# Kernel tuning notes

Measured on AMD Instinct MI355X. Metric: run time of the kernel, lower is better.

Reference implementation:

```python
import jax, jax.numpy as jnp
import numpy as np

N_ATOMS = 4096
N_NEIGH = 32
IN_F = 128
HID = 256
OUT_F = 128
N_SPECIES = 64


def setup_inputs() -> dict:
    key = jax.random.key(0)
    k1, k2, k3, k4, k5, k6 = jax.random.split(key, 6)
    # kaiming-uniform-ish init scales (exact init doesn't matter for correctness testing)
    s1 = 1.0 / np.sqrt(IN_F)
    s2 = 1.0 / np.sqrt(HID)
    return {
        "features": jax.random.normal(k1, (N_ATOMS, N_NEIGH, IN_F), dtype=jnp.float32),
        "species_idx": jax.random.randint(k2, (N_ATOMS,), 0, N_SPECIES, dtype=jnp.int64 if jax.config.jax_enable_x64 else jnp.int32),
        "W1": jax.random.uniform(k3, (N_SPECIES, HID, IN_F), jnp.float32, -s1, s1),
        "b1": jax.random.uniform(k4, (N_SPECIES, HID), jnp.float32, -s1, s1),
        "W2": jax.random.uniform(k5, (N_SPECIES, OUT_F, HID), jnp.float32, -s2, s2),
        "b2": jax.random.uniform(k6, (N_SPECIES, OUT_F), jnp.float32, -s2, s2),
    }


def reference(features, species_idx, W1, b1, W2, b2):
    # Per-atom species-conditioned 2-layer MLP with SiLU after the hidden layer.
    # features: (A, N, in); W[idx]: (A, out, in) gathered per atom (as in torch W[idx]).
    x = jnp.einsum("ani,ahi->anh", features, W1[species_idx]) + b1[species_idx][:, None, :]
    x = jax.nn.silu(x)
    x = jnp.einsum("anh,aoh->ano", x, W2[species_idx]) + b2[species_idx][:, None, :]
    return x  # (A, N, out)
```

## Files before the change

kernel.cpp:

```cpp
#include <hip/hip_runtime.h>

typedef __attribute__((ext_vector_type(8))) short short8;
typedef __attribute__((ext_vector_type(4))) float f32x4;

#define N_ATOMS 4096
#define N_NEIGH 32
#define IN_F 128
#define HID 256
#define OUT_F 128
#define N_SPECIES 64

__device__ __forceinline__ unsigned short f2bf(float f) {
  unsigned u = __float_as_uint(f);
  u += 0x7FFF + ((u >> 16) & 1);
  return (unsigned short)(u >> 16);
}
struct HL { short h, l; };
__device__ __forceinline__ HL split2(float v) {
  unsigned u = __float_as_uint(v);
  float lo = v - __uint_as_float(u & 0xFFFF0000u);
  HL o;
  o.h = (short)(u >> 16);
  o.l = (short)(__float_as_uint(lo) >> 16);
  return o;
}

__global__ __launch_bounds__(256) void prep_kernel(
    const float* __restrict__ W1, const float* __restrict__ W2,
    const int* __restrict__ sp_idx,
    unsigned short* __restrict__ w1h, unsigned short* __restrict__ w2h,
    int* __restrict__ atom_order, int* __restrict__ sp_off, int* __restrict__ sp_cnt) {
  const int t = threadIdx.x;
  if (blockIdx.x == 0) {
    __shared__ int cnt[N_SPECIES], off[N_SPECIES], cur[N_SPECIES];
    if (t < N_SPECIES) cnt[t] = 0;
    __syncthreads();
    for (int a = t; a < N_ATOMS; a += 256) atomicAdd(&cnt[sp_idx[a]], 1);
    __syncthreads();
    if (t == 0) {
      int o = 0;
      for (int s = 0; s < N_SPECIES; ++s) { off[s] = o; cur[s] = o; o += cnt[s]; }
    }
    __syncthreads();
    for (int a = t; a < N_ATOMS; a += 256) {
      int s = sp_idx[a];
      atom_order[atomicAdd(&cur[s], 1)] = a;
    }
    if (t < N_SPECIES) { sp_off[t] = off[t]; sp_cnt[t] = cnt[t]; }
    return;
  }
  const int NV = (N_SPECIES * HID * IN_F) / 4;
  const int nsplit = (gridDim.x - 1) * 256;
  for (int v = (blockIdx.x - 1) * 256 + t; v < 2 * NV; v += nsplit) {
    const float4* src; unsigned short* dh; int j;
    if (v < NV) { src = (const float4*)W1; dh = w1h; j = v; }
    else        { src = (const float4*)W2; dh = w2h; j = v - NV; }
    float4 f = src[j];
    ushort4 h;
    h.x = f2bf(f.x); h.y = f2bf(f.y); h.z = f2bf(f.z); h.w = f2bf(f.w);
    ((ushort4*)dh)[j] = h;
  }
}

__global__ __launch_bounds__(512, 2) void mlp_kernel(
    const float* __restrict__ feat,
    const float* __restrict__ b1g, const float* __restrict__ b2g,
    const unsigned short* __restrict__ w1h, const unsigned short* __restrict__ w2h,
    const int* __restrict__ atom_order, const int* __restrict__ sp_off,
    const int* __restrict__ sp_cnt,
    float* __restrict__ out) {
  extern __shared__ char smem[];
  char* LW1 = smem;
  char* LW2 = smem + 65536;

  const int bid = blockIdx.x;
  const int s = (bid & 7) * 8 + (bid >> 5);
  const int p = (bid >> 3) & 3;
  const int tid = threadIdx.x;
  const int wave = tid >> 6, lane = tid & 63;
  const int q = lane >> 4, r = lane & 15;

  {
    const char* gw1 = (const char*)w1h + (long)s * (HID * IN_F * 2);
    const char* gw2 = (const char*)w2h + (long)s * (OUT_F * HID * 2);
#pragma unroll
    for (int it = 0; it < 8; ++it) {
      const int d = it * 8192 + tid * 16;
      const int h = d >> 8, w = d & 255;
      const int src = h * (IN_F * 2) + (w ^ ((h & 7) << 4));
      __builtin_amdgcn_global_load_lds(
          (const __attribute__((address_space(1))) unsigned int*)(gw1 + src),
          (__attribute__((address_space(3))) unsigned int*)(LW1 + d), 16, 0, 0);
    }
#pragma unroll
    for (int it = 0; it < 8; ++it) {
      const int d = it * 8192 + tid * 16;
      const int o = d >> 9, w = d & 511;
      const int src = o * (HID * 2) + (w ^ ((o & 7) << 4));
      __builtin_amdgcn_global_load_lds(
          (const __attribute__((address_space(1))) unsigned int*)(gw2 + src),
          (__attribute__((address_space(3))) unsigned int*)(LW2 + d), 16, 0, 0);
    }
  }

  const int c = sp_cnt[s], base = sp_off[s];
  const int begin = base + (p * c) / 4;
  const int end   = base + ((p + 1) * c) / 4;

  float b2v[8];
#pragma unroll
  for (int ot = 0; ot < 8; ++ot) b2v[ot] = b2g[s * OUT_F + 16 * ot + r];
  const float* b1s = b1g + s * HID;

  char* lxw = smem + 131072 + wave * 4096;
  const int swz = (r & 7) << 4;

  float4 R[16];
  auto ISSUE = [&](int atom) {
    const float* fb = feat + (long)atom * (N_NEIGH * IN_F);
#pragma unroll
    for (int nt = 0; nt < 2; ++nt)
#pragma unroll
      for (int ks = 0; ks < 4; ++ks) {
        const float* ptr = fb + (16 * nt + r) * IN_F + 32 * ks + 8 * q;
        R[nt * 8 + ks * 2]     = *(const float4*)ptr;
        R[nt * 8 + ks * 2 + 1] = *(const float4*)(ptr + 4);
      }
  };

  int idx = begin + wave;
  int a_cur = 0;
  if (idx < end) { a_cur = atom_order[idx]; ISSUE(a_cur); }

  asm volatile("s_waitcnt vmcnt(0)" ::: "memory");
  __syncthreads();

  while (idx < end) {
    short8 fh[2][4], fl[2][4];
#pragma unroll
    for (int nt = 0; nt < 2; ++nt)
#pragma unroll
      for (int ks = 0; ks < 4; ++ks) {
        float4 v0 = R[nt * 8 + ks * 2];
        float4 v1 = R[nt * 8 + ks * 2 + 1];
        float vv[8] = {v0.x, v0.y, v0.z, v0.w, v1.x, v1.y, v1.z, v1.w};
        short8 h8, l8;
#pragma unroll
        for (int j = 0; j < 8; ++j) {
          HL hl = split2(vv[j]);
          h8[j] = hl.h;
          l8[j] = hl.l;
        }
        fh[nt][ks] = h8;
        fl[nt][ks] = l8;
      }
    const int atom_here = a_cur;
    const int nidx = idx + 8;
    if (nidx < end) { a_cur = atom_order[nidx]; ISSUE(a_cur); }

    f32x4 oacc[2][8] = {};
    for (int hc = 0; hc < 8; ++hc) {
      f32x4 xacc[2][2] = {};
#pragma unroll
      for (int ks = 0; ks < 4; ++ks) {
        const int ib = ((32 * ks + 8 * q) * 2) ^ swz;
#pragma unroll
        for (int ht = 0; ht < 2; ++ht) {
          const int row = 32 * hc + 16 * ht + r;
          short8 bh = *(const short8*)(LW1 + row * 256 + ib);
          xacc[0][ht] = __builtin_amdgcn_mfma_f32_16x16x32_bf16(fh[0][ks], bh, xacc[0][ht], 0, 0, 0);
          xacc[1][ht] = __builtin_amdgcn_mfma_f32_16x16x32_bf16(fh[1][ks], bh, xacc[1][ht], 0, 0, 0);
          xacc[0][ht] = __builtin_amdgcn_mfma_f32_16x16x32_bf16(fl[0][ks], bh, xacc[0][ht], 0, 0, 0);
          xacc[1][ht] = __builtin_amdgcn_mfma_f32_16x16x32_bf16(fl[1][ks], bh, xacc[1][ht], 0, 0, 0);
        }
      }
#pragma unroll
      for (int ht = 0; ht < 2; ++ht) {
        const float b1v = b1s[hc * 32 + 16 * ht + r];
#pragma unroll
        for (int nt = 0; nt < 2; ++nt)
#pragma unroll
          for (int i = 0; i < 4; ++i) {
            const int n = 16 * nt + 4 * q + i;
            float v = xacc[nt][ht][i] + b1v;
            v = v * __builtin_amdgcn_rcpf(1.0f + __expf(-v));
            const int byte = n * 128 + (((16 * ht + r) * 4) ^ ((n & 7) << 4));
            *(float*)(lxw + byte) = v;
          }
      }
      short8 ah[2], al[2];
#pragma unroll
      for (int nt = 0; nt < 2; ++nt) {
        const int n = 16 * nt + r;
        float4 v0 = *(const float4*)(lxw + n * 128 + ((32 * q) ^ swz));
        float4 v1 = *(const float4*)(lxw + n * 128 + ((32 * q + 16) ^ swz));
        float vv[8] = {v0.x, v0.y, v0.z, v0.w, v1.x, v1.y, v1.z, v1.w};
        short8 h8, l8;
#pragma unroll
        for (int j = 0; j < 8; ++j) {
          HL hl = split2(vv[j]);
          h8[j] = hl.h;
          l8[j] = hl.l;
        }
        ah[nt] = h8;
        al[nt] = l8;
      }
      const int kb = ((32 * hc + 8 * q) * 2) ^ swz;
#pragma unroll
      for (int ot = 0; ot < 8; ++ot) {
        const int row = 16 * ot + r;
        short8 bw = *(const short8*)(LW2 + row * 512 + kb);
        oacc[0][ot] = __builtin_amdgcn_mfma_f32_16x16x32_bf16(ah[0], bw, oacc[0][ot], 0, 0, 0);
        oacc[1][ot] = __builtin_amdgcn_mfma_f32_16x16x32_bf16(ah[1], bw, oacc[1][ot], 0, 0, 0);
        oacc[0][ot] = __builtin_amdgcn_mfma_f32_16x16x32_bf16(al[0], bw, oacc[0][ot], 0, 0, 0);
        oacc[1][ot] = __builtin_amdgcn_mfma_f32_16x16x32_bf16(al[1], bw, oacc[1][ot], 0, 0, 0);
      }
    }

    float* ob = out + (long)atom_here * (N_NEIGH * OUT_F);
#pragma unroll
    for (int ot = 0; ot < 8; ++ot)
#pragma unroll
      for (int nt = 0; nt < 2; ++nt)
#pragma unroll
        for (int i = 0; i < 4; ++i) {
          ob[(16 * nt + 4 * q + i) * OUT_F + 16 * ot + r] = oacc[nt][ot][i] + b2v[ot];
        }

    idx = nidx;
  }
}

extern "C" void kernel_launch(void* const* d_in, const int* in_sizes, int n_in,
                              void* d_out, int out_size, void* d_ws, size_t ws_size,
                              hipStream_t stream) {
  const float* feat = (const float*)d_in[0];
  const int* sp     = (const int*)d_in[1];
  const float* W1   = (const float*)d_in[2];
  const float* b1   = (const float*)d_in[3];
  const float* W2   = (const float*)d_in[4];
  const float* b2   = (const float*)d_in[5];
  float* out = (float*)d_out;

  char* ws = (char*)d_ws;
  unsigned short* w1h = (unsigned short*)(ws + 0);
  unsigned short* w2h = (unsigned short*)(ws + 4194304);
  int* atom_order = (int*)(ws + 8388608);
  int* sp_off     = (int*)(ws + 8388608 + 16384);
  int* sp_cnt     = (int*)(ws + 8388608 + 16384 + 256);

  hipFuncSetAttribute((const void*)mlp_kernel,
                      hipFuncAttributeMaxDynamicSharedMemorySize, 163840);

  hipLaunchKernelGGL(prep_kernel, dim3(1025), dim3(256), 0, stream,
                     W1, W2, sp, w1h, w2h, atom_order, sp_off, sp_cnt);
  hipLaunchKernelGGL(mlp_kernel, dim3(256), dim3(512), 163840, stream,
                     feat, b1, b2, w1h, w2h, atom_order, sp_off, sp_cnt, out);
}
```

Baseline: 198.0 us.

## Swap MFMA operand roles to keep hidden activations in registers and coalesce stores

The MFMA operands are transposed so weights become the A operand and features the B operand. The W1 rows are permuted at LDS load time so the layer-1 accumulator layout lines up with the B-operand layout layer 2 needs. This removes the LDS round trip for SiLU activations. Output is staged through a per-wave LDS slab so stores go out as coalesced float4 writes. The software prefetch of the next atom's features into registers is dropped, which exposes global load latency in exchange for fewer registers.

```diff
diff --git a/kernel.cpp b/kernel.cpp
--- a/kernel.cpp
+++ b/kernel.cpp
@@ -86,8 +86,11 @@
 #pragma unroll
     for (int it = 0; it < 8; ++it) {
       const int d = it * 8192 + tid * 16;
-      const int h = d >> 8, w = d & 255;
-      const int src = h * (IN_F * 2) + (w ^ ((h & 7) << 4));
+      const int pos = d >> 8, wb = d & 255;
+      const int pl = pos & 31;
+      const int hl = ((pl >> 2) & 3) * 8 + ((pl >> 4) & 1) * 4 + (pl & 3);
+      const int srow = (pos & ~31) + hl;
+      const int src = srow * (IN_F * 2) + (wb ^ ((pos & 7) << 4));
       __builtin_amdgcn_global_load_lds(
           (const __attribute__((address_space(1))) unsigned int*)(gw1 + src),
           (__attribute__((address_space(3))) unsigned int*)(LW1 + d), 16, 0, 0);
@@ -95,8 +98,8 @@
 #pragma unroll
     for (int it = 0; it < 8; ++it) {
       const int d = it * 8192 + tid * 16;
-      const int o = d >> 9, w = d & 511;
-      const int src = o * (HID * 2) + (w ^ ((o & 7) << 4));
+      const int o = d >> 9, wb = d & 511;
+      const int src = o * (HID * 2) + (wb ^ ((o & 7) << 4));
       __builtin_amdgcn_global_load_lds(
           (const __attribute__((address_space(1))) unsigned int*)(gw2 + src),
           (__attribute__((address_space(3))) unsigned int*)(LW2 + d), 16, 0, 0);
@@ -107,58 +110,42 @@
   const int begin = base + (p * c) / 4;
   const int end   = base + ((p + 1) * c) / 4;
 
-  float b2v[8];
-#pragma unroll
-  for (int ot = 0; ot < 8; ++ot) b2v[ot] = b2g[s * OUT_F + 16 * ot + r];
   const float* b1s = b1g + s * HID;
-
-  char* lxw = smem + 131072 + wave * 4096;
+  const float* b2s = b2g + s * OUT_F;
+  char* slab = smem + 131072 + wave * 4096;
   const int swz = (r & 7) << 4;
-
-  float4 R[16];
-  auto ISSUE = [&](int atom) {
-    const float* fb = feat + (long)atom * (N_NEIGH * IN_F);
-#pragma unroll
-    for (int nt = 0; nt < 2; ++nt)
-#pragma unroll
-      for (int ks = 0; ks < 4; ++ks) {
-        const float* ptr = fb + (16 * nt + r) * IN_F + 32 * ks + 8 * q;
-        R[nt * 8 + ks * 2]     = *(const float4*)ptr;
-        R[nt * 8 + ks * 2 + 1] = *(const float4*)(ptr + 4);
-      }
-  };
-
-  int idx = begin + wave;
-  int a_cur = 0;
-  if (idx < end) { a_cur = atom_order[idx]; ISSUE(a_cur); }
 
   asm volatile("s_waitcnt vmcnt(0)" ::: "memory");
   __syncthreads();
 
-  while (idx < end) {
+  for (int idx = begin + wave; idx < end; idx += 8) {
+    const int atom = atom_order[idx];
+
     short8 fh[2][4], fl[2][4];
-#pragma unroll
-    for (int nt = 0; nt < 2; ++nt)
-#pragma unroll
-      for (int ks = 0; ks < 4; ++ks) {
-        float4 v0 = R[nt * 8 + ks * 2];
-        float4 v1 = R[nt * 8 + ks * 2 + 1];
-        float vv[8] = {v0.x, v0.y, v0.z, v0.w, v1.x, v1.y, v1.z, v1.w};
-        short8 h8, l8;
-#pragma unroll
-        for (int j = 0; j < 8; ++j) {
-          HL hl = split2(vv[j]);
-          h8[j] = hl.h;
-          l8[j] = hl.l;
+    {
+      const float* fb = feat + (long)atom * (N_NEIGH * IN_F);
+#pragma unroll
+      for (int nt = 0; nt < 2; ++nt)
+#pragma unroll
+        for (int ks = 0; ks < 4; ++ks) {
+          const float* ptr = fb + (16 * nt + r) * IN_F + 32 * ks + 8 * q;
+          float4 v0 = *(const float4*)ptr;
+          float4 v1 = *(const float4*)(ptr + 4);
+          float vv[8] = {v0.x, v0.y, v0.z, v0.w, v1.x, v1.y, v1.z, v1.w};
+          short8 h8, l8;
+#pragma unroll
+          for (int j = 0; j < 8; ++j) {
+            HL hl = split2(vv[j]);
+            h8[j] = hl.h;
+            l8[j] = hl.l;
+          }
+          fh[nt][ks] = h8;
+          fl[nt][ks] = l8;
         }
-        fh[nt][ks] = h8;
-        fl[nt][ks] = l8;
-      }
-    const int atom_here = a_cur;
-    const int nidx = idx + 8;
-    if (nidx < end) { a_cur = atom_order[nidx]; ISSUE(a_cur); }
-
-    f32x4 oacc[2][8] = {};
+    }
+
+    f32x4 oacc[8][2] = {};
+
     for (int hc = 0; hc < 8; ++hc) {
       f32x4 xacc[2][2] = {};
 #pragma unroll
@@ -166,68 +153,70 @@
         const int ib = ((32 * ks + 8 * q) * 2) ^ swz;
 #pragma unroll
         for (int ht = 0; ht < 2; ++ht) {
-          const int row = 32 * hc + 16 * ht + r;
-          short8 bh = *(const short8*)(LW1 + row * 256 + ib);
-          xacc[0][ht] = __builtin_amdgcn_mfma_f32_16x16x32_bf16(fh[0][ks], bh, xacc[0][ht], 0, 0, 0);
-          xacc[1][ht] = __builtin_amdgcn_mfma_f32_16x16x32_bf16(fh[1][ks], bh, xacc[1][ht], 0, 0, 0);
-          xacc[0][ht] = __builtin_amdgcn_mfma_f32_16x16x32_bf16(fl[0][ks], bh, xacc[0][ht], 0, 0, 0);
-          xacc[1][ht] = __builtin_amdgcn_mfma_f32_16x16x32_bf16(fl[1][ks], bh, xacc[1][ht], 0, 0, 0);
+          const int pos = 32 * hc + 16 * ht + r;
+          short8 aw = *(const short8*)(LW1 + pos * 256 + ib);
+          xacc[ht][0] = __builtin_amdgcn_mfma_f32_16x16x32_bf16(aw, fh[0][ks], xacc[ht][0], 0, 0, 0);
+          xacc[ht][1] = __builtin_amdgcn_mfma_f32_16x16x32_bf16(aw, fh[1][ks], xacc[ht][1], 0, 0, 0);
+          xacc[ht][0] = __builtin_amdgcn_mfma_f32_16x16x32_bf16(aw, fl[0][ks], xacc[ht][0], 0, 0, 0);
+          xacc[ht][1] = __builtin_amdgcn_mfma_f32_16x16x32_bf16(aw, fl[1][ks], xacc[ht][1], 0, 0, 0);
         }
       }
+      short8 xh[2], xl[2];
 #pragma unroll
       for (int ht = 0; ht < 2; ++ht) {
-        const float b1v = b1s[hc * 32 + 16 * ht + r];
+        const float4 b1c = *(const float4*)(b1s + hc * 32 + 8 * q + 4 * ht);
+        const float bb[4] = {b1c.x, b1c.y, b1c.z, b1c.w};
 #pragma unroll
         for (int nt = 0; nt < 2; ++nt)
 #pragma unroll
-          for (int i = 0; i < 4; ++i) {
-            const int n = 16 * nt + 4 * q + i;
-            float v = xacc[nt][ht][i] + b1v;
+          for (int reg = 0; reg < 4; ++reg) {
+            float v = xacc[ht][nt][reg] + bb[reg];
             v = v * __builtin_amdgcn_rcpf(1.0f + __expf(-v));
-            const int byte = n * 128 + (((16 * ht + r) * 4) ^ ((n & 7) << 4));
-            *(float*)(lxw + byte) = v;
+            HL hl = split2(v);
+            xh[nt][4 * ht + reg] = hl.h;
+            xl[nt][4 * ht + reg] = hl.l;
           }
-      }
-      short8 ah[2], al[2];
-#pragma unroll
-      for (int nt = 0; nt < 2; ++nt) {
-        const int n = 16 * nt + r;
-        float4 v0 = *(const float4*)(lxw + n * 128 + ((32 * q) ^ swz));
-        float4 v1 = *(const float4*)(lxw + n * 128 + ((32 * q + 16) ^ swz));
-        float vv[8] = {v0.x, v0.y, v0.z, v0.w, v1.x, v1.y, v1.z, v1.w};
-        short8 h8, l8;
-#pragma unroll
-        for (int j = 0; j < 8; ++j) {
-          HL hl = split2(vv[j]);
-          h8[j] = hl.h;
-          l8[j] = hl.l;
-        }
-        ah[nt] = h8;
-        al[nt] = l8;
       }
       const int kb = ((32 * hc + 8 * q) * 2) ^ swz;
 #pragma unroll
       for (int ot = 0; ot < 8; ++ot) {
         const int row = 16 * ot + r;
-        short8 bw = *(const short8*)(LW2 + row * 512 + kb);
-        oacc[0][ot] = __builtin_amdgcn_mfma_f32_16x16x32_bf16(ah[0], bw, oacc[0][ot], 0, 0, 0);
-        oacc[1][ot] = __builtin_amdgcn_mfma_f32_16x16x32_bf16(ah[1], bw, oacc[1][ot], 0, 0, 0);
-        oacc[0][ot] = __builtin_amdgcn_mfma_f32_16x16x32_bf16(al[0], bw, oacc[0][ot], 0, 0, 0);
-        oacc[1][ot] = __builtin_amdgcn_mfma_f32_16x16x32_bf16(al[1], bw, oacc[1][ot], 0, 0, 0);
-      }
-    }
-
-    float* ob = out + (long)atom_here * (N_NEIGH * OUT_F);
-#pragma unroll
-    for (int ot = 0; ot < 8; ++ot)
-#pragma unroll
-      for (int nt = 0; nt < 2; ++nt)
-#pragma unroll
-        for (int i = 0; i < 4; ++i) {
-          ob[(16 * nt + 4 * q + i) * OUT_F + 16 * ot + r] = oacc[nt][ot][i] + b2v[ot];
+        short8 aw = *(const short8*)(LW2 + row * 512 + kb);
+        oacc[ot][0] = __builtin_amdgcn_mfma_f32_16x16x32_bf16(aw, xh[0], oacc[ot][0], 0, 0, 0);
+        oacc[ot][1] = __builtin_amdgcn_mfma_f32_16x16x32_bf16(aw, xh[1], oacc[ot][1], 0, 0, 0);
+        oacc[ot][0] = __builtin_amdgcn_mfma_f32_16x16x32_bf16(aw, xl[0], oacc[ot][0], 0, 0, 0);
+        oacc[ot][1] = __builtin_amdgcn_mfma_f32_16x16x32_bf16(aw, xl[1], oacc[ot][1], 0, 0, 0);
+      }
+    }
+
+    float* ob = out + (long)atom * (N_NEIGH * OUT_F);
+#pragma unroll
+    for (int g = 0; g < 4; ++g) {
+#pragma unroll
+      for (int oh = 0; oh < 2; ++oh) {
+        const int ot = 2 * g + oh;
+        const float4 b2c = *(const float4*)(b2s + 16 * ot + 4 * q);
+        const float bb[4] = {b2c.x, b2c.y, b2c.z, b2c.w};
+#pragma unroll
+        for (int nt = 0; nt < 2; ++nt) {
+          f32x4 v;
+#pragma unroll
+          for (int reg = 0; reg < 4; ++reg) v[reg] = oacc[ot][nt][reg] + bb[reg];
+          const int n = 16 * nt + r;
+          const int byte = n * 128 + (((16 * oh + 4 * q) * 4) ^ ((n & 7) << 4));
+          *(f32x4*)(slab + byte) = v;
         }
-
-    idx = nidx;
+      }
+      __builtin_amdgcn_s_waitcnt(0);
+#pragma unroll
+      for (int m = 0; m < 4; ++m) {
+        const int n = m * 8 + (lane >> 3);
+        const int cb = ((lane & 7) * 16) ^ ((n & 7) << 4);
+        float4 v = *(const float4*)(slab + n * 128 + cb);
+        *(float4*)(ob + n * OUT_F + 32 * g + (lane & 7) * 4) = v;
+      }
+      __builtin_amdgcn_s_waitcnt(0);
+    }
   }
 }
 
```

Result: faster. 181.4 us (-8.4%).
